# Kernel tuning notes

Measured on AMD Instinct MI355X. Metric: run time of the kernel, lower is better.

Reference implementation:

```python
import jax, jax.numpy as jnp
import numpy as np

D = 1024
LD = 64
NTR = 8192
NT = 8192
DY = 128

def setup_inputs() -> dict:
    key = jax.random.key(0)
    k1, k2, k3, k4 = jax.random.split(key, 4)
    xtr = jax.random.normal(k1, (NTR, D), dtype=jnp.float32)
    ytr = jax.random.normal(k2, (NTR, DY), dtype=jnp.float32)
    xt = jax.random.normal(k3, (NT, D), dtype=jnp.float32)
    A = jax.random.normal(k4, (D, LD), dtype=jnp.float32) / (D ** 0.5)
    return {"xtr": xtr, "ytr": ytr, "xt": xt, "A": A}

def reference(xtr, ytr, xt, A):
    # mean-center both train and test features with the train mean
    mu = jnp.mean(xtr, axis=0, keepdims=True)          # [1, d]
    qtr = (xtr - mu) @ A                                # [Ntr, ld]
    qt = (xt - mu) @ A                                  # [Nt, ld]
    scores = jnp.einsum('nl,ml->nm', qt, qtr)           # [Nt, Ntr]
    E = jax.nn.softmax(scores, axis=1)                  # row-wise softmax over train points
    return E @ ytr                                      # [Nt, dy]
```

## Files before the change

kernel.cpp:

```cpp
#include <hip/hip_runtime.h>
#include <hip/hip_bf16.h>

#define D    1024
#define LD   64
#define NTR  8192
#define NT   8192
#define DY   128

#define SHIFT 40.0f
#define NCHUNK 8
#define CHUNK (NTR / NCHUNK)

typedef __attribute__((ext_vector_type(8))) short bf16x8;
typedef __attribute__((ext_vector_type(4))) short short4_;
typedef __attribute__((ext_vector_type(4))) float f4;

static __device__ __forceinline__ short f2bf(float f) {
    __hip_bfloat16 h = __float2bfloat16(f);
    short s; __builtin_memcpy(&s, &h, 2); return s;
}
static __device__ __forceinline__ float bf2f(short s) {
    __hip_bfloat16 h; __builtin_memcpy(&h, &s, 2); return __bfloat162float(h);
}

static __device__ __forceinline__ void gload_lds16(const void* g, void* l) {
    __builtin_amdgcn_global_load_lds(
        (const __attribute__((address_space(1))) unsigned int*)g,
        (__attribute__((address_space(3))) unsigned int*)l,
        16, 0, 0);
}

__global__ __launch_bounds__(256) void prep_all(const float* __restrict__ A,
                                                const float* __restrict__ ytr,
                                                short* __restrict__ AThi,
                                                short* __restrict__ ATlo,
                                                short* __restrict__ vtile) {
    __shared__ float tile[64][65];
    int b = blockIdx.x;
    if (b < 64) {
        int k = b * 16 + (threadIdx.x >> 4);
        int c0 = (threadIdx.x & 15) * 4;
        f4 a = *(const f4*)&A[(long)k * LD + c0];
        #pragma unroll
        for (int j = 0; j < 4; ++j) {
            int c = c0 + j;
            short hi = f2bf(a[j]);
            AThi[(long)c * D + k] = hi;
            ATlo[(long)c * D + k] = f2bf(a[j] - bf2f(hi));
        }
    } else {
        int bz = b - 64;
        int t0 = (bz & 127) * 64;
        int d0 = (bz >> 7) * 64;
        int c = threadIdx.x & 63;
        int r4 = threadIdx.x >> 6;
        #pragma unroll
        for (int i = 0; i < 16; ++i) {
            int r = i * 4 + r4;
            tile[r][c] = ytr[(long)(t0 + r) * DY + d0 + c];
        }
        __syncthreads();
        #pragma unroll
        for (int i = 0; i < 16; ++i) {
            int r = i * 4 + r4;
            int t = t0 + c;
            int dy = d0 + r;
            long idx = (long)(t >> 5) * 4096 + (long)dy * 32
                     + ((((t >> 3) & 3) ^ (dy & 3)) << 3) + (t & 7);
            vtile[idx] = f2bf(tile[c][r]);
        }
    }
}

__global__ __launch_bounds__(256) void proj_mfma(const float* __restrict__ xt,
                                                 const float* __restrict__ xtr,
                                                 const short* __restrict__ AThi,
                                                 const short* __restrict__ ATlo,
                                                 short* __restrict__ qt_hi,
                                                 short* __restrict__ qt_lo,
                                                 short* __restrict__ ktr_hi,
                                                 short* __restrict__ ktr_lo) {
    __shared__ __align__(16) float xbuf[2][1024];

    int tid = threadIdx.x;
    int wave = tid >> 6;
    int lane = tid & 63;
    int quad = lane >> 4;
    int l16 = lane & 15;

    int b = blockIdx.x;
    bool is_test = b < (NT / 16);
    int row0 = (is_test ? b : b - NT / 16) * 16;
    const float* x = is_test ? xt : xtr;

    int lr = wave * 4 + (lane >> 4);
    int cg = (lane & 15) ^ (lr & 7);
    const float* xsrc = x + (long)(row0 + lr) * D + cg * 4;
    float* ldst = &xbuf[0][wave * 256];

    const short* bhrow = AThi + (long)(wave * 16 + l16) * D + quad * 8;
    const short* blrow = ATlo + (long)(wave * 16 + l16) * D + quad * 8;

    f4 acc = (f4){0.f, 0.f, 0.f, 0.f};

    int pr0 = ((quad * 2) ^ (l16 & 7)) * 4;
    int pr1 = (((quad * 2) | 1) ^ (l16 & 7)) * 4;

    gload_lds16(xsrc, ldst);
    __syncthreads();

    #pragma unroll 1
    for (int s = 0; s < 16; ++s) {
        int cur = s & 1;
        if (s < 15)
            gload_lds16(xsrc + (s + 1) * 64, &xbuf[cur ^ 1][wave * 256]);

        const float* xrow = &xbuf[cur][l16 * 64];
        bf16x8 ah[2], al[2];
        #pragma unroll
        for (int h = 0; h < 2; ++h) {
            f4 v0 = *(const f4*)(xrow + h * 32 + pr0);
            f4 v1 = *(const f4*)(xrow + h * 32 + pr1);
            #pragma unroll
            for (int e = 0; e < 4; ++e) {
                short hi0 = f2bf(v0[e]);
                short hi1 = f2bf(v1[e]);
                ah[h][e]     = hi0;
                ah[h][e + 4] = hi1;
                al[h][e]     = f2bf(v0[e] - bf2f(hi0));
                al[h][e + 4] = f2bf(v1[e] - bf2f(hi1));
            }
        }
        int k0 = s * 64;
        bf16x8 bh0 = *(const bf16x8*)(bhrow + k0);
        bf16x8 bh1 = *(const bf16x8*)(bhrow + k0 + 32);
        bf16x8 bl0 = *(const bf16x8*)(blrow + k0);
        bf16x8 bl1 = *(const bf16x8*)(blrow + k0 + 32);
        acc = __builtin_amdgcn_mfma_f32_16x16x32_bf16(ah[0], bh0, acc, 0, 0, 0);
        acc = __builtin_amdgcn_mfma_f32_16x16x32_bf16(al[0], bh0, acc, 0, 0, 0);
        acc = __builtin_amdgcn_mfma_f32_16x16x32_bf16(ah[0], bl0, acc, 0, 0, 0);
        acc = __builtin_amdgcn_mfma_f32_16x16x32_bf16(ah[1], bh1, acc, 0, 0, 0);
        acc = __builtin_amdgcn_mfma_f32_16x16x32_bf16(al[1], bh1, acc, 0, 0, 0);
        acc = __builtin_amdgcn_mfma_f32_16x16x32_bf16(ah[1], bl1, acc, 0, 0, 0);

        __syncthreads();
    }


    int col = wave * 16 + l16;
    #pragma unroll
    for (int r = 0; r < 4; ++r) {
        int grow = row0 + quad * 4 + r;
        float qv = acc[r];
        short hi = f2bf(qv);
        short lo = f2bf(qv - bf2f(hi));
        if (is_test) {
            qt_hi[(long)grow * LD + col] = hi;
            qt_lo[(long)grow * LD + col] = lo;
        } else {
            int tl = grow & 31;
            long idx = (long)(grow >> 5) * 2048 + tl * 64
                     + ((((col >> 3) ^ (tl & 7))) << 3) + (col & 7);
            ktr_hi[idx] = hi;
            ktr_lo[idx] = lo;
        }
    }
}

__global__ __launch_bounds__(256) void muA_kernel(const short* __restrict__ ktr_hi,
                                                  const short* __restrict__ ktr_lo,
                                                  float* __restrict__ muA) {
    __shared__ float red[4][64];
    int l = threadIdx.x & 63;
    int g = threadIdx.x >> 6;
    float s = 0.f;
    #pragma unroll 2
    for (int tt = 0; tt < 4; ++tt) {
        long tb = (long)(blockIdx.x * 4 + tt) * 2048;
        #pragma unroll
        for (int tl = g * 8; tl < g * 8 + 8; ++tl) {
            long idx = tb + tl * 64 + ((((l >> 3) ^ (tl & 7))) << 3) + (l & 7);
            s += bf2f(ktr_hi[idx]) + bf2f(ktr_lo[idx]);
        }
    }
    red[g][l] = s;
    __syncthreads();
    if (threadIdx.x < 64)
        atomicAdd(&muA[l], (red[0][l] + red[1][l] + red[2][l] + red[3][l]) *
                               (1.0f / (float)NTR));
}

__global__ __launch_bounds__(256) void c_kernel(const short* __restrict__ ktr_hi,
                                                const short* __restrict__ ktr_lo,
                                                const float* __restrict__ muA,
                                                float* __restrict__ cc) {
    int t = blockIdx.x * 256 + threadIdx.x;
    int tl = t & 31;
    long rb = (long)(t >> 5) * 2048 + tl * 64;
    float s = SHIFT;
    #pragma unroll
    for (int c = 0; c < 8; ++c) {
        int pos = (c ^ (tl & 7)) << 3;
        bf16x8 h8 = *(const bf16x8*)&ktr_hi[rb + pos];
        bf16x8 l8 = *(const bf16x8*)&ktr_lo[rb + pos];
        f4 m0 = *(const f4*)&muA[c * 8];
        f4 m1 = *(const f4*)&muA[c * 8 + 4];
        #pragma unroll
        for (int j = 0; j < 4; ++j) {
            s += (bf2f(h8[j]) + bf2f(l8[j])) * m0[j];
            s += (bf2f(h8[j + 4]) + bf2f(l8[j + 4])) * m1[j];
        }
    }
    cc[t] = s;
}

__global__ __launch_bounds__(256, 2) void flash_kernel(const short* __restrict__ qt_hi,
                                                       const short* __restrict__ qt_lo,
                                                       const short* __restrict__ ksw_hi,
                                                       const short* __restrict__ ksw_lo,
                                                       const short* __restrict__ vtile,
                                                       const float* __restrict__ cc,
                                                       float* __restrict__ Opart,
                                                       float* __restrict__ Lpart) {
    __shared__ __align__(16) short kbh[2][2048];
    __shared__ __align__(16) short kbl[2][2048];
    __shared__ __align__(16) short vbuf[2][4096];
    __shared__ __align__(16) short ptile[4][1280];

    int tid = threadIdx.x;
    int wave = tid >> 6;
    int lane = tid & 63;
    int quad = lane >> 4;
    int l16 = lane & 15;

    int kc = blockIdx.x & 7;
    int qi = blockIdx.x >> 3;
    int q0w = qi * 128 + wave * 32;
    int tile0 = kc * 32;
    int kc0 = kc * CHUNK;

    int soff = wave * 512 + lane * 8;
    int ldso = wave * 512;

    bf16x8 qh[2][2], ql[2][2];
    #pragma unroll
    for (int rt = 0; rt < 2; ++rt) {
        const short* qrh = qt_hi + (long)(q0w + rt * 16 + l16) * LD + quad * 8;
        const short* qrl = qt_lo + (long)(q0w + rt * 16 + l16) * LD + quad * 8;
        qh[rt][0] = *(const bf16x8*)qrh;
        qh[rt][1] = *(const bf16x8*)(qrh + 32);
        ql[rt][0] = *(const bf16x8*)qrl;
        ql[rt][1] = *(const bf16x8*)(qrl + 32);
    }

    bf16x8 onef;
    #pragma unroll
    for (int i = 0; i < 8; ++i) onef[i] = (short)0x3F80;

    f4 Ov[2][8];
    f4 Lv[2];
    #pragma unroll
    for (int rt = 0; rt < 2; ++rt) {
        Lv[rt] = (f4){0.f, 0.f, 0.f, 0.f};
        #pragma unroll
        for (int jt = 0; jt < 8; ++jt) Ov[rt][jt] = (f4){0.f, 0.f, 0.f, 0.f};
    }

    short* myp = &ptile[wave][0];
    const int p0 = ((quad ^ (l16 & 7)) << 3);
    const int pv = ((quad ^ (l16 & 3)) << 3);

    gload_lds16(ksw_hi + (long)tile0 * 2048 + soff, &kbh[0][ldso]);
    gload_lds16(ksw_lo + (long)tile0 * 2048 + soff, &kbl[0][ldso]);
    gload_lds16(vtile + (long)tile0 * 4096 + soff, &vbuf[0][ldso]);
    gload_lds16(vtile + (long)tile0 * 4096 + 2048 + soff, &vbuf[0][2048 + ldso]);
    __syncthreads();

    #pragma unroll 1
    for (int it = 0; it < 32; ++it) {
        int cur = it & 1;

        f4 cv[2];
        #pragma unroll
        for (int tt = 0; tt < 2; ++tt)
            cv[tt] = *(const f4*)&cc[kc0 + it * 32 + tt * 16 + quad * 4];

        if (it < 31) {
            int nb = cur ^ 1;
            long tb = (long)(tile0 + it + 1);
            gload_lds16(ksw_hi + tb * 2048 + soff, &kbh[nb][ldso]);
            gload_lds16(ksw_lo + tb * 2048 + soff, &kbl[nb][ldso]);
            gload_lds16(vtile + tb * 4096 + soff, &vbuf[nb][ldso]);
            gload_lds16(vtile + tb * 4096 + 2048 + soff, &vbuf[nb][2048 + ldso]);
        }

        bf16x8 kh[2][2], kl[2][2];
        #pragma unroll
        for (int tt = 0; tt < 2; ++tt) {
            int rb = (tt * 16 + l16) * 64;
            kh[tt][0] = *(const bf16x8*)&kbh[cur][rb + p0];
            kh[tt][1] = *(const bf16x8*)&kbh[cur][rb + (p0 ^ 32)];
            kl[tt][0] = *(const bf16x8*)&kbl[cur][rb + p0];
            kl[tt][1] = *(const bf16x8*)&kbl[cur][rb + (p0 ^ 32)];
        }

        f4 s[2][2];
        #pragma unroll
        for (int rt = 0; rt < 2; ++rt) {
            #pragma unroll
            for (int tt = 0; tt < 2; ++tt) {
                f4 a = (f4){0.f, 0.f, 0.f, 0.f};
                a = __builtin_amdgcn_mfma_f32_16x16x32_bf16(kh[tt][0], qh[rt][0], a, 0, 0, 0);
                a = __builtin_amdgcn_mfma_f32_16x16x32_bf16(kh[tt][0], ql[rt][0], a, 0, 0, 0);
                a = __builtin_amdgcn_mfma_f32_16x16x32_bf16(kh[tt][1], qh[rt][1], a, 0, 0, 0);
                a = __builtin_amdgcn_mfma_f32_16x16x32_bf16(kh[tt][1], ql[rt][1], a, 0, 0, 0);
                a = __builtin_amdgcn_mfma_f32_16x16x32_bf16(kl[tt][0], qh[rt][0], a, 0, 0, 0);
                a = __builtin_amdgcn_mfma_f32_16x16x32_bf16(kl[tt][1], qh[rt][1], a, 0, 0, 0);
                s[rt][tt] = a;
            }
        }

        #pragma unroll
        for (int rt = 0; rt < 2; ++rt) {
            #pragma unroll
            for (int tt = 0; tt < 2; ++tt) {
                short4_ p4;
                p4[0] = f2bf(__expf(s[rt][tt][0] - cv[tt][0]));
                p4[1] = f2bf(__expf(s[rt][tt][1] - cv[tt][1]));
                p4[2] = f2bf(__expf(s[rt][tt][2] - cv[tt][2]));
                p4[3] = f2bf(__expf(s[rt][tt][3] - cv[tt][3]));
                *(short4_*)&myp[(rt * 16 + l16) * 40 + tt * 16 + quad * 4] = p4;
            }
        }

        bf16x8 vf[8];
        #pragma unroll
        for (int jt = 0; jt < 8; ++jt)
            vf[jt] = *(const bf16x8*)&vbuf[cur][(jt * 16 + l16) * 32 + pv];
        #pragma unroll
        for (int rt = 0; rt < 2; ++rt) {
            bf16x8 pf = *(const bf16x8*)&myp[(rt * 16 + l16) * 40 + quad * 8];
            #pragma unroll
            for (int jt = 0; jt < 8; ++jt)
                Ov[rt][jt] = __builtin_amdgcn_mfma_f32_16x16x32_bf16(pf, vf[jt], Ov[rt][jt], 0, 0, 0);
            Lv[rt] = __builtin_amdgcn_mfma_f32_16x16x32_bf16(pf, onef, Lv[rt], 0, 0, 0);
        }

        __syncthreads();
    }

    long ob = (long)kc * NT;
    #pragma unroll
    for (int rt = 0; rt < 2; ++rt) {
        #pragma unroll
        for (int jt = 0; jt < 8; ++jt) {
            #pragma unroll
            for (int r = 0; r < 4; ++r)
                Opart[(ob + q0w + rt * 16 + quad * 4 + r) * DY + jt * 16 + l16] =
                    Ov[rt][jt][r];
        }
        if (l16 == 0) {
            #pragma unroll
            for (int r = 0; r < 4; ++r)
                Lpart[ob + q0w + rt * 16 + quad * 4 + r] = Lv[rt][r];
        }
    }
}

__global__ __launch_bounds__(256) void finalize_kernel(const float* __restrict__ Opart,
                                                       const float* __restrict__ Lpart,
                                                       float* __restrict__ out) {
    long i = ((long)blockIdx.x * 256 + threadIdx.x) * 8;
    long row = i >> 7;
    float L = 0.f;
    f4 a = (f4){0.f, 0.f, 0.f, 0.f};
    f4 b = (f4){0.f, 0.f, 0.f, 0.f};
    #pragma unroll
    for (int kc = 0; kc < NCHUNK; ++kc) {
        L += Lpart[(long)kc * NT + row];
        const float* p = &Opart[((long)kc * NT) * DY + i];
        a += *(const f4*)p;
        b += *(const f4*)(p + 4);
    }
    float linv = 1.0f / L;
    a *= linv; b *= linv;
    *(f4*)&out[i] = a;
    *(f4*)&out[i + 4] = b;
}

extern "C" void kernel_launch(void* const* d_in, const int* in_sizes, int n_in,
                              void* d_out, int out_size, void* d_ws, size_t ws_size,
                              hipStream_t stream) {
    const float* xtr = (const float*)d_in[0];
    const float* ytr = (const float*)d_in[1];
    const float* xt  = (const float*)d_in[2];
    const float* A   = (const float*)d_in[3];
    float* out = (float*)d_out;

    char* w = (char*)d_ws;
    float* muA   = (float*)w; w += 4096;
    float* cc    = (float*)w; w += (size_t)NTR * 4;
    float* Lpart = (float*)w; w += (size_t)NCHUNK * NT * 4;
    float* Opart = (float*)w; w += (size_t)NCHUNK * NT * DY * 4;
    short* AThi  = (short*)w; w += (size_t)LD * D * 2;
    short* ATlo  = (short*)w; w += (size_t)LD * D * 2;
    short* qt_hi  = (short*)w; w += (size_t)NT * LD * 2;
    short* qt_lo  = (short*)w; w += (size_t)NT * LD * 2;
    short* ksw_hi = (short*)w; w += (size_t)NTR * LD * 2;
    short* ksw_lo = (short*)w; w += (size_t)NTR * LD * 2;
    short* vtile  = (short*)w; w += (size_t)DY * NTR * 2;
    (void)ws_size; (void)in_sizes; (void)n_in; (void)out_size;

    hipMemsetAsync(muA, 0, 4096, stream);
    prep_all<<<320, 256, 0, stream>>>(A, ytr, AThi, ATlo, vtile);
    proj_mfma<<<1024, 256, 0, stream>>>(xt, xtr, AThi, ATlo,
                                        qt_hi, qt_lo, ksw_hi, ksw_lo);
    muA_kernel<<<64, 256, 0, stream>>>(ksw_hi, ksw_lo, muA);
    c_kernel<<<32, 256, 0, stream>>>(ksw_hi, ksw_lo, muA, cc);
    flash_kernel<<<512, 256, 0, stream>>>(qt_hi, qt_lo, ksw_hi, ksw_lo, vtile, cc,
                                          Opart, Lpart);
    finalize_kernel<<<(NT * DY) / (256 * 8), 256, 0, stream>>>(Opart, Lpart, out);
}
```

Baseline: 195.4 us.

## Fuse muA reduction into projection, deepen proj stages, double flash query tile

Three changes at once. The projection kernel now stages 128 columns per iteration, which halves the number of barriers. The muA column-mean reduction moves into the projection epilogue using shuffles and atomics, so the separate muA kernel is gone. The flash kernel handles 64 query rows per wave instead of 32, so each loaded K/V tile is reused across twice as many queries, with half the blocks and launch bounds set to one block per CU. The trade-off is higher register pressure from Ov[4][8] and a launch of only 256 blocks, which may underfill the GPU.

Measured after the change: 202.4 us. 1.04x slower.

```diff
diff --git a/kernel.cpp b/kernel.cpp
--- a/kernel.cpp
+++ b/kernel.cpp
@@ -79,8 +79,9 @@
                                                  short* __restrict__ qt_hi,
                                                  short* __restrict__ qt_lo,
                                                  short* __restrict__ ktr_hi,
-                                                 short* __restrict__ ktr_lo) {
-    __shared__ __align__(16) float xbuf[2][1024];
+                                                 short* __restrict__ ktr_lo,
+                                                 float* __restrict__ muA) {
+    __shared__ __align__(16) float xbuf[2][2][1024];
 
     int tid = threadIdx.x;
     int wave = tid >> 6;
@@ -96,7 +97,6 @@
     int lr = wave * 4 + (lane >> 4);
     int cg = (lane & 15) ^ (lr & 7);
     const float* xsrc = x + (long)(row0 + lr) * D + cg * 4;
-    float* ldst = &xbuf[0][wave * 256];
 
     const short* bhrow = AThi + (long)(wave * 16 + l16) * D + quad * 8;
     const short* blrow = ATlo + (long)(wave * 16 + l16) * D + quad * 8;
@@ -106,46 +106,51 @@
     int pr0 = ((quad * 2) ^ (l16 & 7)) * 4;
     int pr1 = (((quad * 2) | 1) ^ (l16 & 7)) * 4;
 
-    gload_lds16(xsrc, ldst);
+    gload_lds16(xsrc, &xbuf[0][0][wave * 256]);
+    gload_lds16(xsrc + 64, &xbuf[0][1][wave * 256]);
     __syncthreads();
 
     #pragma unroll 1
-    for (int s = 0; s < 16; ++s) {
+    for (int s = 0; s < 8; ++s) {
         int cur = s & 1;
-        if (s < 15)
-            gload_lds16(xsrc + (s + 1) * 64, &xbuf[cur ^ 1][wave * 256]);
-
-        const float* xrow = &xbuf[cur][l16 * 64];
-        bf16x8 ah[2], al[2];
-        #pragma unroll
-        for (int h = 0; h < 2; ++h) {
-            f4 v0 = *(const f4*)(xrow + h * 32 + pr0);
-            f4 v1 = *(const f4*)(xrow + h * 32 + pr1);
-            #pragma unroll
-            for (int e = 0; e < 4; ++e) {
-                short hi0 = f2bf(v0[e]);
-                short hi1 = f2bf(v1[e]);
-                ah[h][e]     = hi0;
-                ah[h][e + 4] = hi1;
-                al[h][e]     = f2bf(v0[e] - bf2f(hi0));
-                al[h][e + 4] = f2bf(v1[e] - bf2f(hi1));
+        if (s < 7) {
+            const float* nsrc = xsrc + (s + 1) * 128;
+            gload_lds16(nsrc, &xbuf[cur ^ 1][0][wave * 256]);
+            gload_lds16(nsrc + 64, &xbuf[cur ^ 1][1][wave * 256]);
+        }
+
+        #pragma unroll
+        for (int s2 = 0; s2 < 2; ++s2) {
+            const float* xrow = &xbuf[cur][s2][l16 * 64];
+            bf16x8 ah[2], al[2];
+            #pragma unroll
+            for (int h = 0; h < 2; ++h) {
+                f4 v0 = *(const f4*)(xrow + h * 32 + pr0);
+                f4 v1 = *(const f4*)(xrow + h * 32 + pr1);
+                #pragma unroll
+                for (int e = 0; e < 4; ++e) {
+                    short hi0 = f2bf(v0[e]);
+                    short hi1 = f2bf(v1[e]);
+                    ah[h][e]     = hi0;
+                    ah[h][e + 4] = hi1;
+                    al[h][e]     = f2bf(v0[e] - bf2f(hi0));
+                    al[h][e + 4] = f2bf(v1[e] - bf2f(hi1));
+                }
             }
-        }
-        int k0 = s * 64;
-        bf16x8 bh0 = *(const bf16x8*)(bhrow + k0);
-        bf16x8 bh1 = *(const bf16x8*)(bhrow + k0 + 32);
-        bf16x8 bl0 = *(const bf16x8*)(blrow + k0);
-        bf16x8 bl1 = *(const bf16x8*)(blrow + k0 + 32);
-        acc = __builtin_amdgcn_mfma_f32_16x16x32_bf16(ah[0], bh0, acc, 0, 0, 0);
-        acc = __builtin_amdgcn_mfma_f32_16x16x32_bf16(al[0], bh0, acc, 0, 0, 0);
-        acc = __builtin_amdgcn_mfma_f32_16x16x32_bf16(ah[0], bl0, acc, 0, 0, 0);
-        acc = __builtin_amdgcn_mfma_f32_16x16x32_bf16(ah[1], bh1, acc, 0, 0, 0);
-        acc = __builtin_amdgcn_mfma_f32_16x16x32_bf16(al[1], bh1, acc, 0, 0, 0);
-        acc = __builtin_amdgcn_mfma_f32_16x16x32_bf16(ah[1], bl1, acc, 0, 0, 0);
-
+            int k0 = s * 128 + s2 * 64;
+            bf16x8 bh0 = *(const bf16x8*)(bhrow + k0);
+            bf16x8 bh1 = *(const bf16x8*)(bhrow + k0 + 32);
+            bf16x8 bl0 = *(const bf16x8*)(blrow + k0);
+            bf16x8 bl1 = *(const bf16x8*)(blrow + k0 + 32);
+            acc = __builtin_amdgcn_mfma_f32_16x16x32_bf16(ah[0], bh0, acc, 0, 0, 0);
+            acc = __builtin_amdgcn_mfma_f32_16x16x32_bf16(al[0], bh0, acc, 0, 0, 0);
+            acc = __builtin_amdgcn_mfma_f32_16x16x32_bf16(ah[0], bl0, acc, 0, 0, 0);
+            acc = __builtin_amdgcn_mfma_f32_16x16x32_bf16(ah[1], bh1, acc, 0, 0, 0);
+            acc = __builtin_amdgcn_mfma_f32_16x16x32_bf16(al[1], bh1, acc, 0, 0, 0);
+            acc = __builtin_amdgcn_mfma_f32_16x16x32_bf16(ah[1], bl1, acc, 0, 0, 0);
+        }
         __syncthreads();
     }
-
 
     int col = wave * 16 + l16;
     #pragma unroll
@@ -165,29 +170,13 @@
             ktr_lo[idx] = lo;
         }
     }
-}
-
-__global__ __launch_bounds__(256) void muA_kernel(const short* __restrict__ ktr_hi,
-                                                  const short* __restrict__ ktr_lo,
-                                                  float* __restrict__ muA) {
-    __shared__ float red[4][64];
-    int l = threadIdx.x & 63;
-    int g = threadIdx.x >> 6;
-    float s = 0.f;
-    #pragma unroll 2
-    for (int tt = 0; tt < 4; ++tt) {
-        long tb = (long)(blockIdx.x * 4 + tt) * 2048;
-        #pragma unroll
-        for (int tl = g * 8; tl < g * 8 + 8; ++tl) {
-            long idx = tb + tl * 64 + ((((l >> 3) ^ (tl & 7))) << 3) + (l & 7);
-            s += bf2f(ktr_hi[idx]) + bf2f(ktr_lo[idx]);
-        }
-    }
-    red[g][l] = s;
-    __syncthreads();
-    if (threadIdx.x < 64)
-        atomicAdd(&muA[l], (red[0][l] + red[1][l] + red[2][l] + red[3][l]) *
-                               (1.0f / (float)NTR));
+
+    if (!is_test) {
+        float s = acc[0] + acc[1] + acc[2] + acc[3];
+        s += __shfl_xor(s, 16);
+        s += __shfl_xor(s, 32);
+        if (quad == 0) atomicAdd(&muA[col], s * (1.0f / (float)NTR));
+    }
 }
 
 __global__ __launch_bounds__(256) void c_kernel(const short* __restrict__ ktr_hi,
@@ -214,7 +203,7 @@
     cc[t] = s;
 }
 
-__global__ __launch_bounds__(256, 2) void flash_kernel(const short* __restrict__ qt_hi,
+__global__ __launch_bounds__(256, 1) void flash_kernel(const short* __restrict__ qt_hi,
                                                        const short* __restrict__ qt_lo,
                                                        const short* __restrict__ ksw_hi,
                                                        const short* __restrict__ ksw_lo,
@@ -225,7 +214,7 @@
     __shared__ __align__(16) short kbh[2][2048];
     __shared__ __align__(16) short kbl[2][2048];
     __shared__ __align__(16) short vbuf[2][4096];
-    __shared__ __align__(16) short ptile[4][1280];
+    __shared__ __align__(16) short ptile[4][64 * 40];
 
     int tid = threadIdx.x;
     int wave = tid >> 6;
@@ -235,16 +224,16 @@
 
     int kc = blockIdx.x & 7;
     int qi = blockIdx.x >> 3;
-    int q0w = qi * 128 + wave * 32;
+    int q0w = qi * 256 + wave * 64;
     int tile0 = kc * 32;
     int kc0 = kc * CHUNK;
 
     int soff = wave * 512 + lane * 8;
     int ldso = wave * 512;
 
-    bf16x8 qh[2][2], ql[2][2];
-    #pragma unroll
-    for (int rt = 0; rt < 2; ++rt) {
+    bf16x8 qh[4][2], ql[4][2];
+    #pragma unroll
+    for (int rt = 0; rt < 4; ++rt) {
         const short* qrh = qt_hi + (long)(q0w + rt * 16 + l16) * LD + quad * 8;
         const short* qrl = qt_lo + (long)(q0w + rt * 16 + l16) * LD + quad * 8;
         qh[rt][0] = *(const bf16x8*)qrh;
@@ -257,10 +246,10 @@
     #pragma unroll
     for (int i = 0; i < 8; ++i) onef[i] = (short)0x3F80;
 
-    f4 Ov[2][8];
-    f4 Lv[2];
-    #pragma unroll
-    for (int rt = 0; rt < 2; ++rt) {
+    f4 Ov[4][8];
+    f4 Lv[4];
+    #pragma unroll
+    for (int rt = 0; rt < 4; ++rt) {
         Lv[rt] = (f4){0.f, 0.f, 0.f, 0.f};
         #pragma unroll
         for (int jt = 0; jt < 8; ++jt) Ov[rt][jt] = (f4){0.f, 0.f, 0.f, 0.f};
@@ -304,9 +293,9 @@
             kl[tt][1] = *(const bf16x8*)&kbl[cur][rb + (p0 ^ 32)];
         }
 
-        f4 s[2][2];
-        #pragma unroll
-        for (int rt = 0; rt < 2; ++rt) {
+        #pragma unroll
+        for (int rt = 0; rt < 4; ++rt) {
+            f4 s[2];
             #pragma unroll
             for (int tt = 0; tt < 2; ++tt) {
                 f4 a = (f4){0.f, 0.f, 0.f, 0.f};
@@ -316,42 +305,40 @@
                 a = __builtin_amdgcn_mfma_f32_16x16x32_bf16(kh[tt][1], ql[rt][1], a, 0, 0, 0);
                 a = __builtin_amdgcn_mfma_f32_16x16x32_bf16(kl[tt][0], qh[rt][0], a, 0, 0, 0);
                 a = __builtin_amdgcn_mfma_f32_16x16x32_bf16(kl[tt][1], qh[rt][1], a, 0, 0, 0);
-                s[rt][tt] = a;
+                s[tt] = a;
             }
-        }
-
-        #pragma unroll
-        for (int rt = 0; rt < 2; ++rt) {
             #pragma unroll
             for (int tt = 0; tt < 2; ++tt) {
                 short4_ p4;
-                p4[0] = f2bf(__expf(s[rt][tt][0] - cv[tt][0]));
-                p4[1] = f2bf(__expf(s[rt][tt][1] - cv[tt][1]));
-                p4[2] = f2bf(__expf(s[rt][tt][2] - cv[tt][2]));
-                p4[3] = f2bf(__expf(s[rt][tt][3] - cv[tt][3]));
+                p4[0] = f2bf(__expf(s[tt][0] - cv[tt][0]));
+                p4[1] = f2bf(__expf(s[tt][1] - cv[tt][1]));
+                p4[2] = f2bf(__expf(s[tt][2] - cv[tt][2]));
+                p4[3] = f2bf(__expf(s[tt][3] - cv[tt][3]));
                 *(short4_*)&myp[(rt * 16 + l16) * 40 + tt * 16 + quad * 4] = p4;
             }
         }
 
-        bf16x8 vf[8];
-        #pragma unroll
-        for (int jt = 0; jt < 8; ++jt)
-            vf[jt] = *(const bf16x8*)&vbuf[cur][(jt * 16 + l16) * 32 + pv];
-        #pragma unroll
-        for (int rt = 0; rt < 2; ++rt) {
-            bf16x8 pf = *(const bf16x8*)&myp[(rt * 16 + l16) * 40 + quad * 8];
-            #pragma unroll
-            for (int jt = 0; jt < 8; ++jt)
-                Ov[rt][jt] = __builtin_amdgcn_mfma_f32_16x16x32_bf16(pf, vf[jt], Ov[rt][jt], 0, 0, 0);
-            Lv[rt] = __builtin_amdgcn_mfma_f32_16x16x32_bf16(pf, onef, Lv[rt], 0, 0, 0);
-        }
+        bf16x8 pf[4];
+        #pragma unroll
+        for (int rt = 0; rt < 4; ++rt)
+            pf[rt] = *(const bf16x8*)&myp[(rt * 16 + l16) * 40 + quad * 8];
+        #pragma unroll
+        for (int jt = 0; jt < 8; ++jt) {
+            bf16x8 vf = *(const bf16x8*)&vbuf[cur][(jt * 16 + l16) * 32 + pv];
+            #pragma unroll
+            for (int rt = 0; rt < 4; ++rt)
+                Ov[rt][jt] = __builtin_amdgcn_mfma_f32_16x16x32_bf16(pf[rt], vf, Ov[rt][jt], 0, 0, 0);
+        }
+        #pragma unroll
+        for (int rt = 0; rt < 4; ++rt)
+            Lv[rt] = __builtin_amdgcn_mfma_f32_16x16x32_bf16(pf[rt], onef, Lv[rt], 0, 0, 0);
 
         __syncthreads();
     }
 
     long ob = (long)kc * NT;
     #pragma unroll
-    for (int rt = 0; rt < 2; ++rt) {
+    for (int rt = 0; rt < 4; ++rt) {
         #pragma unroll
         for (int jt = 0; jt < 8; ++jt) {
             #pragma unroll
@@ -414,10 +401,9 @@
     hipMemsetAsync(muA, 0, 4096, stream);
     prep_all<<<320, 256, 0, stream>>>(A, ytr, AThi, ATlo, vtile);
     proj_mfma<<<1024, 256, 0, stream>>>(xt, xtr, AThi, ATlo,
-                                        qt_hi, qt_lo, ksw_hi, ksw_lo);
-    muA_kernel<<<64, 256, 0, stream>>>(ksw_hi, ksw_lo, muA);
+                                        qt_hi, qt_lo, ksw_hi, ksw_lo, muA);
     c_kernel<<<32, 256, 0, stream>>>(ksw_hi, ksw_lo, muA, cc);
-    flash_kernel<<<512, 256, 0, stream>>>(qt_hi, qt_lo, ksw_hi, ksw_lo, vtile, cc,
+    flash_kernel<<<256, 256, 0, stream>>>(qt_hi, qt_lo, ksw_hi, ksw_lo, vtile, cc,
                                           Opart, Lpart);
     finalize_kernel<<<(NT * DY) / (256 * 8), 256, 0, stream>>>(Opart, Lpart, out);
 }
```
